# Kernel optimization log

Measured on AMD Instinct MI355X. Metric: run time of the kernel, lower is better.

## Reference

```python
import jax, jax.numpy as jnp
import numpy as np

B, C, H, W = 2, 64, 256, 256
CQ = C // 8    # query/key channels
CR = C // 16   # ShareChannelAttention reduction


def _conv1x1(x, w, b):
    # x: [B,C,H,W], w: [O,C], b: [O]  (1x1 conv == per-pixel linear)
    return jnp.einsum('bchw,oc->bohw', x, w) + b[None, :, None, None]


def _criss_cross(q, k, v):
    # q,k: [B,CQ,H,W], v: [B,C,H,W]; row+column attention with -inf on the
    # H-diagonal, softmax over concatenated H+W energies.
    Hh = q.shape[2]
    eH = jnp.einsum('bchw,bcgw->bhwg', q, k)                 # column (over h') energies
    eH = jnp.where(jnp.eye(Hh, dtype=bool)[:, None, :], -jnp.inf, eH)
    eW = jnp.einsum('bchw,bchv->bhwv', q, k)                 # row (over w') energies
    att = jax.nn.softmax(jnp.concatenate([eH, eW], axis=-1), axis=-1)  # [B,H,W,H+W]
    aH, aW = att[..., :Hh], att[..., Hh:]
    outH = jnp.einsum('bhwg,bcgw->bchw', aH, v)
    outW = jnp.einsum('bhwv,bchv->bchw', aW, v)
    return outH + outW


def _shareca(xa, xb, w1, b1, w2, b2):
    s = xa + xb
    def mlp(p):
        return _conv1x1(jax.nn.relu(_conv1x1(p, w1, b1)), w2, b2)
    gate = jax.nn.sigmoid(mlp(s.mean(axis=(2, 3), keepdims=True)) +
                          mlp(s.max(axis=(2, 3), keepdims=True)))
    return gate * s  # gate*xa + gate*xb


def _bn_relu(x, scale, bias):
    # BatchNorm2d in training mode (batch statistics, biased variance), eps=1e-5
    m = x.mean(axis=(0, 2, 3), keepdims=True)
    v = x.var(axis=(0, 2, 3), keepdims=True)
    xn = (x - m) * jax.lax.rsqrt(v + 1e-5)
    return jax.nn.relu(xn * scale[None, :, None, None] + bias[None, :, None, None])


def setup_inputs() -> dict:
    key = jax.random.key(0)
    ks = jax.random.split(key, 32)
    def n(k, shape, s=0.05):
        return jax.random.normal(k, shape, dtype=jnp.float32) * s
    inp = {
        'x1': n(ks[0], (B, C, H, W), 1.0),
        'x2': n(ks[1], (B, C, H, W), 1.0),
        'wq1': n(ks[2], (CQ, C)), 'bq1': n(ks[3], (CQ,)),
        'wq2': n(ks[4], (CQ, C)), 'bq2': n(ks[5], (CQ,)),
        'wk1': n(ks[6], (CQ, C)), 'bk1': n(ks[7], (CQ,)),
        'wk2': n(ks[8], (CQ, C)), 'bk2': n(ks[9], (CQ,)),
        'wv1': n(ks[10], (C, C)), 'bv1': n(ks[11], (C,)),
        'wv2': n(ks[12], (C, C)), 'bv2': n(ks[13], (C,)),
        'gamma1': n(ks[14], (1,), 0.5), 'gamma2': n(ks[15], (1,), 0.5),
        'sc1_w1': n(ks[16], (CR, C)), 'sc1_b1': n(ks[17], (CR,)),
        'sc1_w2': n(ks[18], (C, CR)), 'sc1_b2': n(ks[19], (C,)),
        'sc2_w1': n(ks[20], (CR, C)), 'sc2_b1': n(ks[21], (CR,)),
        'sc2_w2': n(ks[22], (C, CR)), 'sc2_b2': n(ks[23], (C,)),
        'bn1_scale': jnp.ones((C,), jnp.float32), 'bn1_bias': n(ks[24], (C,)),
        'bn2_scale': jnp.ones((C,), jnp.float32), 'bn2_bias': n(ks[25], (C,)),
    }
    return inp


def reference(x1, x2, wq1, bq1, wq2, bq2, wk1, bk1, wk2, bk2,
              wv1, bv1, wv2, bv2, gamma1, gamma2,
              sc1_w1, sc1_b1, sc1_w2, sc1_b2,
              sc2_w1, sc2_b1, sc2_w2, sc2_b2,
              bn1_scale, bn1_bias, bn2_scale, bn2_bias):
    q1 = _conv1x1(x1, wq1, bq1); q2 = _conv1x1(x2, wq2, bq2)
    k1 = _conv1x1(x1, wk1, bk1); k2 = _conv1x1(x2, wk2, bk2)
    v1 = _conv1x1(x1, wv1, bv1); v2 = _conv1x1(x2, wv2, bv2)
    att1 = _criss_cross(q2, k1, v1)  # out_H_1 + out_W_1
    att2 = _criss_cross(q1, k2, v2)  # out_H_2 + out_W_2
    x_1 = _shareca(gamma2 * att2 + x2, x1, sc1_w1, sc1_b1, sc1_w2, sc1_b2)
    x_2 = _shareca(gamma1 * att1 + x1, x2, sc2_w1, sc2_b1, sc2_w2, sc2_b2)
    out1 = _bn_relu(x_1 + x1, bn1_scale, bn1_bias)
    out2 = _bn_relu(x_2 + x2, bn2_scale, bn2_bias)
    # channel exchange: even channels keep the original input
    mask = (jnp.arange(C) % 2 == 0)[None, :, None, None]
    return jnp.where(mask, x1, out1), jnp.where(mask, x2, out2)
```

## Files before the change

kernel.cpp:

```cpp
#include <hip/hip_runtime.h>
#include <hip/hip_bf16.h>
#include <cstdint>
#include <cstddef>

typedef unsigned short bf16t;
typedef __attribute__((ext_vector_type(8))) short bf16x8;
typedef __attribute__((ext_vector_type(4))) float f32x4;

__device__ __forceinline__ unsigned short f2bf(float f) {
    unsigned u = __float_as_uint(f);
    u += 0x7fffu + ((u >> 16) & 1u);
    return (unsigned short)(u >> 16);
}
__device__ __forceinline__ float bf2f(unsigned short h) {
    return __uint_as_float(((unsigned)h) << 16);
}
__device__ __forceinline__ float bflo(unsigned u) { return __uint_as_float(u << 16); }
__device__ __forceinline__ float bfhi(unsigned u) { return __uint_as_float(u & 0xffff0000u); }
__device__ __forceinline__ unsigned pk2(float a, float b) {
    __hip_bfloat162 h = __float22bfloat162_rn(make_float2(a, b));
    return *(unsigned*)&h;
}

__device__ __forceinline__ unsigned fenc(float f) {
    unsigned u = __float_as_uint(f);
    return (u & 0x80000000u) ? ~u : (u | 0x80000000u);
}
__device__ __forceinline__ float fdec(unsigned u) {
    return __uint_as_float((u & 0x80000000u) ? (u ^ 0x80000000u) : ~u);
}

#define HW 65536

struct ConvArgs {
    const float* x[2];
    const float* wq[2]; const float* bq[2];
    const float* wk[2]; const float* bk[2];
    const float* wv[2]; const float* bv[2];
    bf16t* q[2]; bf16t* k[2]; bf16t* v[2];
    unsigned* zeroR;
};

__global__ __launch_bounds__(256) void conv_qkv(ConvArgs A)
{
    const int t = threadIdx.x;
    const int z = blockIdx.z;
    const int s = z >> 1, b = z & 1;
    if (z == 0 && blockIdx.x == 0 && blockIdx.y == 0) {
#pragma unroll
        for (int i = 0; i < 6; i++) A.zeroR[t + i * 256] = 0u;
    }
    const int h = blockIdx.y * 4 + (t >> 6);
    const int w = blockIdx.x * 64 + (t & 63);
    const int pix = h * 256 + w;

    const float* wq = A.wq[s]; const float* wk = A.wk[s]; const float* wv = A.wv[s];
    float qa[8], ka[8], va[64];
#pragma unroll
    for (int o = 0; o < 8; o++) { qa[o] = A.bq[s][o]; ka[o] = A.bk[s][o]; }
#pragma unroll
    for (int o = 0; o < 64; o++) va[o] = A.bv[s][o];

    const float* xb = A.x[s] + (size_t)b * 64 * HW + pix;
    for (int c = 0; c < 64; c++) {
        const float xv = xb[(size_t)c * HW];
#pragma unroll
        for (int o = 0; o < 8; o++) { qa[o] += wq[o * 64 + c] * xv; ka[o] += wk[o * 64 + c] * xv; }
#pragma unroll
        for (int o = 0; o < 64; o++) va[o] += wv[o * 64 + c] * xv;
    }
    bf16t* qo = A.q[s] + (size_t)b * 8 * HW + pix;
    bf16t* ko = A.k[s] + (size_t)b * 8 * HW + pix;
    bf16t* vo = A.v[s] + (size_t)b * 64 * HW + pix;
#pragma unroll
    for (int o = 0; o < 8; o++) { qo[(size_t)o * HW] = f2bf(qa[o]); ko[(size_t)o * HW] = f2bf(ka[o]); }
#pragma unroll
    for (int o = 0; o < 64; o++) vo[(size_t)o * HW] = f2bf(va[o]);
}

__global__ __launch_bounds__(256) void transpose16(const bf16t* __restrict__ in, bf16t* __restrict__ out)
{
    __shared__ bf16t tile[64][68];
    const size_t zo = (size_t)blockIdx.z * HW;
    const int i0 = blockIdx.y * 64, j0 = blockIdx.x * 64;
    const int lc = threadIdx.x & 63, rg = threadIdx.x >> 6;
#pragma unroll
    for (int rr = 0; rr < 16; rr++) {
        int row = rg * 16 + rr;
        tile[row][lc] = in[zo + (size_t)(i0 + row) * 256 + j0 + lc];
    }
    __syncthreads();
#pragma unroll
    for (int rr = 0; rr < 16; rr++) {
        int row = rg * 16 + rr;
        out[zo + (size_t)(j0 + row) * 256 + i0 + lc] = tile[lc][row];
    }
}

struct RowccArgs {
    const bf16t* q[4]; const bf16t* k[4]; const bf16t* v[4];
    bf16t* o[4]; float* so[4];
};

__global__ __launch_bounds__(256, 3) void rowcc_mfma(RowccArgs P)
{
    __shared__ __align__(16) char smem[54272];
    bf16t* vs = (bf16t*)smem;
    bf16t* ps = (bf16t*)(smem + 33792);

    const int t = threadIdx.x;
    const int r = blockIdx.x, b = blockIdx.y, z = blockIdx.z;
    const bool mask = (z < 2);
    const int lane = t & 63, wv = t >> 6, quad = lane >> 4, l16 = lane & 15;
    const int wband = wv * 64;

    const bf16t* qp = P.q[z];
    const bf16t* kp = P.k[z];
    const bf16t* vp = P.v[z];

    const size_t vb = (size_t)b * 64 * HW + (size_t)r * 256;
#pragma unroll
    for (int i = 0; i < 8; i++) {
        const int qd = i * 256 + t;
        const int c = qd >> 5, jc = (qd & 31) * 8;
        *(uint4*)&vs[c * 264 + jc] = *(const uint4*)&vp[vb + (size_t)c * HW + jc];
    }

    const bf16x8 zfr = {0, 0, 0, 0, 0, 0, 0, 0};
    bf16x8 qfr[4] = {zfr, zfr, zfr, zfr};
    const size_t rowb = (size_t)b * 8 * HW + (size_t)r * 256;
    if (quad == 0) {
#pragma unroll
        for (int wt = 0; wt < 4; wt++) {
            const int w_g = wband + wt * 16 + l16;
#pragma unroll
            for (int ch = 0; ch < 8; ch++)
                qfr[wt][ch] = (short)qp[rowb + (size_t)ch * HW + w_g];
        }
    }

    const f32x4 z4 = {0.f, 0.f, 0.f, 0.f};
    f32x4 acc[4][4];
#pragma unroll
    for (int i = 0; i < 4; i++)
#pragma unroll
        for (int j = 0; j < 4; j++) acc[i][j] = z4;
    float s_t[4] = {0.f, 0.f, 0.f, 0.f};

    bf16x8 kcur[2] = {zfr, zfr};
    if (quad == 0) {
#pragma unroll
        for (int jtile = 0; jtile < 2; jtile++)
#pragma unroll
            for (int ch = 0; ch < 8; ch++)
                kcur[jtile][ch] = (short)kp[rowb + (size_t)ch * HW + jtile * 16 + l16];
    }

    __syncthreads();

    for (int jt = 0; jt < 8; jt++) {
        const int j0 = jt * 32;
        f32x4 e[4][2];
#pragma unroll
        for (int wt = 0; wt < 4; wt++)
#pragma unroll
            for (int jtile = 0; jtile < 2; jtile++)
                e[wt][jtile] = __builtin_amdgcn_mfma_f32_16x16x32_bf16(kcur[jtile], qfr[wt], z4, 0, 0, 0);

        bf16x8 knext[2] = {zfr, zfr};
        if (jt < 7 && quad == 0) {
            const int jn = (jt + 1) * 32;
#pragma unroll
            for (int jtile = 0; jtile < 2; jtile++)
#pragma unroll
                for (int ch = 0; ch < 8; ch++)
                    knext[jtile][ch] = (short)kp[rowb + (size_t)ch * HW + jn + jtile * 16 + l16];
        }

        if (mask && (jt >> 1) == wv) {
#pragma unroll
            for (int wt = 0; wt < 4; wt++) {
                const int w_g = wband + wt * 16 + l16;
#pragma unroll
                for (int jtile = 0; jtile < 2; jtile++)
#pragma unroll
                    for (int rr = 0; rr < 4; rr++)
                        if (j0 + jtile * 16 + quad * 4 + rr == w_g) e[wt][jtile][rr] = -3.0e38f;
            }
        }

#pragma unroll
        for (int wt = 0; wt < 4; wt++) {
#pragma unroll
            for (int jtile = 0; jtile < 2; jtile++) {
                const float p0 = __expf(e[wt][jtile][0]);
                const float p1 = __expf(e[wt][jtile][1]);
                const float p2 = __expf(e[wt][jtile][2]);
                const float p3 = __expf(e[wt][jtile][3]);
                s_t[wt] += (p0 + p1) + (p2 + p3);
                uint2 u; u.x = pk2(p0, p1); u.y = pk2(p2, p3);
                *(uint2*)&ps[(wband + wt * 16 + l16) * 40 + jtile * 16 + quad * 4] = u;
            }
        }

        bf16x8 afr[4], bfr[4];
#pragma unroll
        for (int wt = 0; wt < 4; wt++)
            afr[wt] = *(const bf16x8*)&ps[(wband + wt * 16 + l16) * 40 + quad * 8];
#pragma unroll
        for (int ct = 0; ct < 4; ct++)
            bfr[ct] = *(const bf16x8*)&vs[(ct * 16 + l16) * 264 + j0 + quad * 8];
#pragma unroll
        for (int wt = 0; wt < 4; wt++)
#pragma unroll
            for (int ct = 0; ct < 4; ct++)
                acc[wt][ct] = __builtin_amdgcn_mfma_f32_16x16x32_bf16(afr[wt], bfr[ct], acc[wt][ct], 0, 0, 0);

        kcur[0] = knext[0]; kcur[1] = knext[1];
    }

#pragma unroll
    for (int wt = 0; wt < 4; wt++) {
        float s = s_t[wt];
        s += __shfl_xor(s, 16, 64);
        s += __shfl_xor(s, 32, 64);
        s_t[wt] = s;
    }
    if (quad == 0) {
#pragma unroll
        for (int wt = 0; wt < 4; wt++) {
            const int w_g = wband + wt * 16 + l16;
            if (mask)
                P.so[z][(size_t)b * HW + w_g * 256 + r] = s_t[wt];
            else
                P.so[z][(size_t)b * HW + r * 256 + w_g] = s_t[wt];
        }
    }

    __syncthreads();
    bf16t* o_lds = (bf16t*)smem;
#pragma unroll
    for (int wt = 0; wt < 4; wt++) {
        const int w0 = wband + wt * 16 + quad * 4;
#pragma unroll
        for (int ct = 0; ct < 4; ct++) {
            const int c = ct * 16 + l16;
            uint2 u;
            u.x = pk2(acc[wt][ct][0], acc[wt][ct][1]);
            u.y = pk2(acc[wt][ct][2], acc[wt][ct][3]);
            *(uint2*)&o_lds[c * 264 + w0] = u;
        }
    }
    __syncthreads();
    bf16t* ob = P.o[z] + (size_t)b * 64 * HW + (size_t)r * 256;
#pragma unroll
    for (int i = 0; i < 8; i++) {
        const int qd = i * 256 + t;
        const int c = qd >> 5, w8 = (qd & 31) * 8;
        *(uint4*)&ob[(size_t)c * HW + w8] = *(const uint4*)&o_lds[c * 264 + w8];
    }
}

__global__ __launch_bounds__(256) void combine_reduce(
    const bf16t* __restrict__ oH1, const bf16t* __restrict__ oW1,
    const bf16t* __restrict__ oH2, const bf16t* __restrict__ oW2,
    const float* __restrict__ sH1, const float* __restrict__ sW1,
    const float* __restrict__ sH2, const float* __restrict__ sW2,
    const float* __restrict__ x1, const float* __restrict__ x2,
    const float* __restrict__ gamma1, const float* __restrict__ gamma2,
    bf16t* __restrict__ s1, bf16t* __restrict__ s2,
    float* __restrict__ accum, unsigned* __restrict__ accmax)
{
    const int t = threadIdx.x, chunk = blockIdx.x, c = blockIdx.y, b = blockIdx.z;
    const float g1v = gamma1[0], g2v = gamma2[0];
    const size_t cb = ((size_t)(b * 64 + c)) * HW;
    const size_t pb = (size_t)b * HW;

    float pS1 = 0, pSS1 = 0, pSX1 = 0, pX1 = 0, pXX1 = 0, pM1 = -3e38f;
    float pS2 = 0, pSS2 = 0, pSX2 = 0, pX2 = 0, pXX2 = 0, pM2 = -3e38f;

    for (int i = 0; i < 16; i++) {
        const int pidx = chunk * 4096 + i * 256 + t;
        const float inv1 = 1.f / (sH1[pb + pidx] + sW1[pb + pidx]);
        const float inv2 = 1.f / (sH2[pb + pidx] + sW2[pb + pidx]);
        const float a1 = (bf2f(oH1[cb + pidx]) + bf2f(oW1[cb + pidx])) * inv1;
        const float a2 = (bf2f(oH2[cb + pidx]) + bf2f(oW2[cb + pidx])) * inv2;
        const float x1v = x1[cb + pidx], x2v = x2[cb + pidx];
        const float s1v = g2v * a2 + x2v + x1v;
        const float s2v = g1v * a1 + x1v + x2v;
        s1[cb + pidx] = f2bf(s1v);
        s2[cb + pidx] = f2bf(s2v);
        pS1 += s1v; pSS1 += s1v * s1v; pSX1 += s1v * x1v; pX1 += x1v; pXX1 += x1v * x1v; pM1 = fmaxf(pM1, s1v);
        pS2 += s2v; pSS2 += s2v * s2v; pSX2 += s2v * x2v; pX2 += x2v; pXX2 += x2v * x2v; pM2 = fmaxf(pM2, s2v);
    }

    __shared__ float wred[12][4];
    float vals[12] = {pS1, pSS1, pSX1, pX1, pXX1, pM1, pS2, pSS2, pSX2, pX2, pXX2, pM2};
    const int lane = t & 63, wave = t >> 6;
#pragma unroll
    for (int iv = 0; iv < 12; iv++) {
        float v = vals[iv];
        const bool isMax = (iv == 5 || iv == 11);
#pragma unroll
        for (int off = 32; off > 0; off >>= 1) {
            const float o = __shfl_down(v, off, 64);
            v = isMax ? fmaxf(v, o) : (v + o);
        }
        if (lane == 0) wred[iv][wave] = v;
    }
    __syncthreads();
    if (t < 12) {
        const bool isMax = (t == 5 || t == 11);
        float v = wred[t][0];
        for (int i = 1; i < 4; i++) v = isMax ? fmaxf(v, wred[t][i]) : (v + wred[t][i]);
        const int stream = (t >= 6) ? 1 : 0;
        const int kk = t - stream * 6;
        if (kk == 5) atomicMax(&accmax[(stream * 2 + b) * 64 + c], fenc(v));
        else atomicAdd(&accum[((stream * 2 + b) * 64 + c) * 5 + kk], v);
    }
}

__global__ __launch_bounds__(256) void gates_bn(
    const float* __restrict__ accum, const unsigned* __restrict__ accmax,
    const float* __restrict__ sc1_w1, const float* __restrict__ sc1_b1,
    const float* __restrict__ sc1_w2, const float* __restrict__ sc1_b2,
    const float* __restrict__ sc2_w1, const float* __restrict__ sc2_b1,
    const float* __restrict__ sc2_w2, const float* __restrict__ sc2_b2,
    const float* __restrict__ bn1_scale, const float* __restrict__ bn1_bias,
    const float* __restrict__ bn2_scale, const float* __restrict__ bn2_bias,
    float* __restrict__ gates, float* __restrict__ AB)
{
    const int t = threadIdx.x;
    const int stream = t >> 7, b = (t >> 6) & 1, c = t & 63;
    __shared__ float meanS[256], maxS[256], e1S[256], e2S[256];

    const float S = accum[t * 5 + 0], SS = accum[t * 5 + 1], SX = accum[t * 5 + 2];
    const float X = accum[t * 5 + 3], XX = accum[t * 5 + 4];
    meanS[t] = S * (1.f / 65536.f);
    maxS[t] = fdec(accmax[t]);
    __syncthreads();

    const float* w1 = stream ? sc2_w1 : sc1_w1;
    const float* b1 = stream ? sc2_b1 : sc1_b1;
    const float* w2 = stream ? sc2_w2 : sc1_w2;
    const float* b2 = stream ? sc2_b2 : sc1_b2;
    float om = b2[c], ox = b2[c];
    const int base = stream * 128 + b * 64;
#pragma unroll
    for (int r = 0; r < 4; r++) {
        float hm = b1[r], hx = b1[r];
        for (int cc = 0; cc < 64; cc++) {
            hm += w1[r * 64 + cc] * meanS[base + cc];
            hx += w1[r * 64 + cc] * maxS[base + cc];
        }
        hm = fmaxf(hm, 0.f); hx = fmaxf(hx, 0.f);
        om += w2[c * 4 + r] * hm;
        ox += w2[c * 4 + r] * hx;
    }
    const float gate = 1.f / (1.f + __expf(-(om + ox)));
    gates[t] = gate;
    e1S[t] = gate * S + X;
    e2S[t] = gate * gate * SS + 2.f * gate * SX + XX;
    __syncthreads();
    if (b == 0) {
        const float sumY = e1S[t] + e1S[t + 64];
        const float sumY2 = e2S[t] + e2S[t + 64];
        const float meanY = sumY * (1.f / 131072.f);
        const float varY = sumY2 * (1.f / 131072.f) - meanY * meanY;
        const float sc = stream ? bn2_scale[c] : bn1_scale[c];
        const float bi = stream ? bn2_bias[c] : bn1_bias[c];
        const float A = sc * rsqrtf(varY + 1e-5f);
        AB[stream * 128 + c] = A;
        AB[stream * 128 + 64 + c] = bi - meanY * A;
    }
}

__global__ __launch_bounds__(256) void finalize(
    const bf16t* __restrict__ s1, const bf16t* __restrict__ s2,
    const float* __restrict__ x1, const float* __restrict__ x2,
    const float* __restrict__ gates, const float* __restrict__ AB,
    float* __restrict__ out)
{
    const size_t tid = (size_t)blockIdx.x * 256 + threadIdx.x;
    const size_t idx = tid * 4;
    const int b = (int)(idx >> 22);
    const int c = (int)((idx >> 16) & 63);
    const bool odd = (c & 1) != 0;
    const float g1 = gates[b * 64 + c], g2 = gates[128 + b * 64 + c];
    const float A1 = AB[c], B1 = AB[64 + c], A2 = AB[128 + c], B2 = AB[192 + c];

    const uint2 su1 = *(const uint2*)(s1 + idx);
    const uint2 su2 = *(const uint2*)(s2 + idx);
    const float4 x1v = *(const float4*)(x1 + idx);
    const float4 x2v = *(const float4*)(x2 + idx);
    float s1f[4] = {bflo(su1.x), bfhi(su1.x), bflo(su1.y), bfhi(su1.y)};
    float s2f[4] = {bflo(su2.x), bfhi(su2.x), bflo(su2.y), bfhi(su2.y)};
    float xa[4] = {x1v.x, x1v.y, x1v.z, x1v.w};
    float xb[4] = {x2v.x, x2v.y, x2v.z, x2v.w};
    float o1[4], o2[4];
#pragma unroll
    for (int j = 0; j < 4; j++) {
        const float y1 = g1 * s1f[j] + xa[j];
        const float y2 = g2 * s2f[j] + xb[j];
        o1[j] = odd ? fmaxf(A1 * y1 + B1, 0.f) : xa[j];
        o2[j] = odd ? fmaxf(A2 * y2 + B2, 0.f) : xb[j];
    }
    *(float4*)(out + idx) = make_float4(o1[0], o1[1], o1[2], o1[3]);
    *(float4*)(out + 8388608 + idx) = make_float4(o2[0], o2[1], o2[2], o2[3]);
}

extern "C" void kernel_launch(void* const* d_in, const int* in_sizes, int n_in,
                              void* d_out, int out_size, void* d_ws, size_t ws_size,
                              hipStream_t stream) {
    (void)in_sizes; (void)n_in; (void)out_size; (void)ws_size;
    const float* x1 = (const float*)d_in[0];
    const float* x2 = (const float*)d_in[1];
    const float* wq1 = (const float*)d_in[2];  const float* bq1 = (const float*)d_in[3];
    const float* wq2 = (const float*)d_in[4];  const float* bq2 = (const float*)d_in[5];
    const float* wk1 = (const float*)d_in[6];  const float* bk1 = (const float*)d_in[7];
    const float* wk2 = (const float*)d_in[8];  const float* bk2 = (const float*)d_in[9];
    const float* wv1 = (const float*)d_in[10]; const float* bv1 = (const float*)d_in[11];
    const float* wv2 = (const float*)d_in[12]; const float* bv2 = (const float*)d_in[13];
    const float* gamma1 = (const float*)d_in[14];
    const float* gamma2 = (const float*)d_in[15];
    const float* sc1_w1 = (const float*)d_in[16]; const float* sc1_b1 = (const float*)d_in[17];
    const float* sc1_w2 = (const float*)d_in[18]; const float* sc1_b2 = (const float*)d_in[19];
    const float* sc2_w1 = (const float*)d_in[20]; const float* sc2_b1 = (const float*)d_in[21];
    const float* sc2_w2 = (const float*)d_in[22]; const float* sc2_b2 = (const float*)d_in[23];
    const float* bn1_scale = (const float*)d_in[24]; const float* bn1_bias = (const float*)d_in[25];
    const float* bn2_scale = (const float*)d_in[26]; const float* bn2_bias = (const float*)d_in[27];

    char* p = (char*)d_ws;
    const size_t SZ_QK = 2097152;
    const size_t SZ_V = 16777216;
    const size_t SZ_ST = 524288;

    bf16t* q1 = (bf16t*)(p + 0 * SZ_QK);
    bf16t* k1 = (bf16t*)(p + 1 * SZ_QK);
    bf16t* q2 = (bf16t*)(p + 2 * SZ_QK);
    bf16t* k2 = (bf16t*)(p + 3 * SZ_QK);
    bf16t* v1 = (bf16t*)(p + 4 * SZ_QK);
    bf16t* v2 = (bf16t*)(p + 4 * SZ_QK + SZ_V);
    size_t off = 4 * SZ_QK + 2 * SZ_V;
    bf16t* q1T = (bf16t*)(p + off + 0 * SZ_QK);
    bf16t* k1T = (bf16t*)(p + off + 1 * SZ_QK);
    bf16t* q2T = (bf16t*)(p + off + 2 * SZ_QK);
    bf16t* k2T = (bf16t*)(p + off + 3 * SZ_QK);
    bf16t* v1T = (bf16t*)(p + off + 4 * SZ_QK);
    bf16t* v2T = (bf16t*)(p + off + 4 * SZ_QK + SZ_V);
    off += 4 * SZ_QK + 2 * SZ_V;
    bf16t* oH1T = (bf16t*)(p + off); off += SZ_V;
    bf16t* oH2T = (bf16t*)(p + off); off += SZ_V;
    bf16t* oW1 = (bf16t*)(p + off); off += SZ_V;
    bf16t* oW2 = (bf16t*)(p + off); off += SZ_V;
    float* sH1 = (float*)(p + off); off += SZ_ST;
    float* sH2 = (float*)(p + off); off += SZ_ST;
    float* sW1 = (float*)(p + off); off += SZ_ST;
    float* sW2 = (float*)(p + off); off += SZ_ST;
    float* accum = (float*)(p + off);
    unsigned* accmax = (unsigned*)(p + off + 5120);
    float* gates = (float*)(p + off + 6144);
    float* AB = (float*)(p + off + 7168);

    bf16t* oH1 = v1T;
    bf16t* oH2 = v2T;
    bf16t* s1 = oH1T;
    bf16t* s2 = oH2T;

    ConvArgs CA;
    CA.x[0] = x1; CA.x[1] = x2;
    CA.wq[0] = wq1; CA.wq[1] = wq2; CA.bq[0] = bq1; CA.bq[1] = bq2;
    CA.wk[0] = wk1; CA.wk[1] = wk2; CA.bk[0] = bk1; CA.bk[1] = bk2;
    CA.wv[0] = wv1; CA.wv[1] = wv2; CA.bv[0] = bv1; CA.bv[1] = bv2;
    CA.q[0] = q1; CA.q[1] = q2; CA.k[0] = k1; CA.k[1] = k2;
    CA.v[0] = v1; CA.v[1] = v2;
    CA.zeroR = (unsigned*)accum;
    conv_qkv<<<dim3(4, 64, 4), 256, 0, stream>>>(CA);

    transpose16<<<dim3(4, 4, 320), 256, 0, stream>>>(q1, q1T);

    RowccArgs RA;
    RA.q[0] = q2T; RA.k[0] = k1T; RA.v[0] = v1T; RA.o[0] = oH1T; RA.so[0] = sH1;
    RA.q[1] = q1T; RA.k[1] = k2T; RA.v[1] = v2T; RA.o[1] = oH2T; RA.so[1] = sH2;
    RA.q[2] = q2;  RA.k[2] = k1;  RA.v[2] = v1;  RA.o[2] = oW1;  RA.so[2] = sW1;
    RA.q[3] = q1;  RA.k[3] = k2;  RA.v[3] = v2;  RA.o[3] = oW2;  RA.so[3] = sW2;
    rowcc_mfma<<<dim3(256, 2, 4), 256, 0, stream>>>(RA);

    transpose16<<<dim3(4, 4, 256), 256, 0, stream>>>(oH1T, oH1);

    combine_reduce<<<dim3(16, 64, 2), 256, 0, stream>>>(
        oH1, oW1, oH2, oW2, sH1, sW1, sH2, sW2, x1, x2, gamma1, gamma2,
        s1, s2, accum, accmax);

    gates_bn<<<1, 256, 0, stream>>>(accum, accmax,
                                    sc1_w1, sc1_b1, sc1_w2, sc1_b2,
                                    sc2_w1, sc2_b1, sc2_w2, sc2_b2,
                                    bn1_scale, bn1_bias, bn2_scale, bn2_bias,
                                    gates, AB);

    finalize<<<8192, 256, 0, stream>>>(s1, s2, x1, x2, gates, AB, (float*)d_out);
}
```

Before: 366.5 us.

## Compute QKV 1x1 convolutions with bf16 MFMA via LDS-staged inputs

The QKV projection kernel moves from scalar FMA loops, where each thread held 80 fp32 accumulators, to bf16 MFMA 16x16x32 tiles. Each block loads 256 pixels by 64 channels of x, converts them to bf16 and stages them in LDS as the A operand. The weights become B fragments covering the 80 output channels (q, k, v). This cuts the FP32 ALU work and register pressure, but rounds x and the weights to bf16 before accumulation, which lowers precision.

```diff
diff --git a/kernel.cpp b/kernel.cpp
--- a/kernel.cpp
+++ b/kernel.cpp
@@ -20,6 +20,9 @@
 __device__ __forceinline__ unsigned pk2(float a, float b) {
     __hip_bfloat162 h = __float22bfloat162_rn(make_float2(a, b));
     return *(unsigned*)&h;
+}
+__device__ __forceinline__ bf16x8 mk8(unsigned a, unsigned b, unsigned c, unsigned d) {
+    union { uint4 u; bf16x8 v; } cv; cv.u = make_uint4(a, b, c, d); return cv.v;
 }
 
 __device__ __forceinline__ unsigned fenc(float f) {
@@ -43,39 +46,89 @@
 
 __global__ __launch_bounds__(256) void conv_qkv(ConvArgs A)
 {
+    __shared__ __align__(16) bf16t Xlds[256 * 68];
+
     const int t = threadIdx.x;
     const int z = blockIdx.z;
     const int s = z >> 1, b = z & 1;
-    if (z == 0 && blockIdx.x == 0 && blockIdx.y == 0) {
+    if (z == 0 && blockIdx.x == 0) {
 #pragma unroll
         for (int i = 0; i < 6; i++) A.zeroR[t + i * 256] = 0u;
     }
-    const int h = blockIdx.y * 4 + (t >> 6);
-    const int w = blockIdx.x * 64 + (t & 63);
-    const int pix = h * 256 + w;
-
-    const float* wq = A.wq[s]; const float* wk = A.wk[s]; const float* wv = A.wv[s];
-    float qa[8], ka[8], va[64];
-#pragma unroll
-    for (int o = 0; o < 8; o++) { qa[o] = A.bq[s][o]; ka[o] = A.bk[s][o]; }
-#pragma unroll
-    for (int o = 0; o < 64; o++) va[o] = A.bv[s][o];
-
-    const float* xb = A.x[s] + (size_t)b * 64 * HW + pix;
-    for (int c = 0; c < 64; c++) {
-        const float xv = xb[(size_t)c * HW];
-#pragma unroll
-        for (int o = 0; o < 8; o++) { qa[o] += wq[o * 64 + c] * xv; ka[o] += wk[o * 64 + c] * xv; }
-#pragma unroll
-        for (int o = 0; o < 64; o++) va[o] += wv[o * 64 + c] * xv;
-    }
-    bf16t* qo = A.q[s] + (size_t)b * 8 * HW + pix;
-    bf16t* ko = A.k[s] + (size_t)b * 8 * HW + pix;
-    bf16t* vo = A.v[s] + (size_t)b * 64 * HW + pix;
-#pragma unroll
-    for (int o = 0; o < 8; o++) { qo[(size_t)o * HW] = f2bf(qa[o]); ko[(size_t)o * HW] = f2bf(ka[o]); }
-#pragma unroll
-    for (int o = 0; o < 64; o++) vo[(size_t)o * HW] = f2bf(va[o]);
+    const int lane = t & 63, wv = t >> 6, quad = lane >> 4, l16 = lane & 15;
+    const int px0 = blockIdx.x * 256;
+
+    const float* xp = A.x[s] + (size_t)b * 64 * HW + px0 + t;
+    {
+        unsigned xw[32];
+#pragma unroll
+        for (int c = 0; c < 32; c++)
+            xw[c] = pk2(xp[(size_t)(2 * c) * HW], xp[(size_t)(2 * c + 1) * HW]);
+#pragma unroll
+        for (int g = 0; g < 16; g++)
+            *(uint2*)&Xlds[t * 68 + g * 4] = make_uint2(xw[2 * g], xw[2 * g + 1]);
+    }
+
+    bf16x8 bfr[5][2];
+    float bo[5];
+    bf16t* obase[5];
+#pragma unroll
+    for (int ot = 0; ot < 5; ot++) {
+        const int o = ot * 16 + l16;
+        const float* wrow;
+        if (o < 8)       { wrow = A.wq[s] + o * 64;        bo[ot] = A.bq[s][o];
+                           obase[ot] = A.q[s] + (size_t)(b * 8 + o) * HW; }
+        else if (o < 16) { wrow = A.wk[s] + (o - 8) * 64;  bo[ot] = A.bk[s][o - 8];
+                           obase[ot] = A.k[s] + (size_t)(b * 8 + o - 8) * HW; }
+        else             { wrow = A.wv[s] + (o - 16) * 64; bo[ot] = A.bv[s][o - 16];
+                           obase[ot] = A.v[s] + (size_t)(b * 64 + o - 16) * HW; }
+#pragma unroll
+        for (int ks = 0; ks < 2; ks++) {
+            const float* wp = wrow + ks * 32 + quad * 8;
+            bfr[ot][ks] = mk8(pk2(wp[0], wp[1]), pk2(wp[2], wp[3]),
+                              pk2(wp[4], wp[5]), pk2(wp[6], wp[7]));
+        }
+    }
+
+    __syncthreads();
+
+    bf16x8 afr[4][2];
+#pragma unroll
+    for (int i = 0; i < 4; i++)
+#pragma unroll
+        for (int ks = 0; ks < 2; ks++) {
+            const int base = (wv * 64 + i * 16 + l16) * 68 + ks * 32 + quad * 8;
+            const uint2 lo = *(const uint2*)&Xlds[base];
+            const uint2 hi = *(const uint2*)&Xlds[base + 4];
+            afr[i][ks] = mk8(lo.x, lo.y, hi.x, hi.y);
+        }
+
+    const f32x4 z4 = {0.f, 0.f, 0.f, 0.f};
+    f32x4 acc[4][5];
+#pragma unroll
+    for (int i = 0; i < 4; i++)
+#pragma unroll
+        for (int ot = 0; ot < 5; ot++) acc[i][ot] = z4;
+
+#pragma unroll
+    for (int ks = 0; ks < 2; ks++)
+#pragma unroll
+        for (int i = 0; i < 4; i++)
+#pragma unroll
+            for (int ot = 0; ot < 5; ot++)
+                acc[i][ot] = __builtin_amdgcn_mfma_f32_16x16x32_bf16(afr[i][ks], bfr[ot][ks], acc[i][ot], 0, 0, 0);
+
+#pragma unroll
+    for (int i = 0; i < 4; i++) {
+        const int px = px0 + wv * 64 + i * 16 + quad * 4;
+#pragma unroll
+        for (int ot = 0; ot < 5; ot++) {
+            uint2 u;
+            u.x = pk2(acc[i][ot][0] + bo[ot], acc[i][ot][1] + bo[ot]);
+            u.y = pk2(acc[i][ot][2] + bo[ot], acc[i][ot][3] + bo[ot]);
+            *(uint2*)&obase[ot][px] = u;
+        }
+    }
 }
 
 __global__ __launch_bounds__(256) void transpose16(const bf16t* __restrict__ in, bf16t* __restrict__ out)
@@ -475,7 +528,7 @@
     CA.q[0] = q1; CA.q[1] = q2; CA.k[0] = k1; CA.k[1] = k2;
     CA.v[0] = v1; CA.v[1] = v2;
     CA.zeroR = (unsigned*)accum;
-    conv_qkv<<<dim3(4, 64, 4), 256, 0, stream>>>(CA);
+    conv_qkv<<<dim3(256, 1, 4), 256, 0, stream>>>(CA);
 
     transpose16<<<dim3(4, 4, 320), 256, 0, stream>>>(q1, q1T);
 
```

Result: faster. 323.4 us (-11.8%).
